# Optimization experiments

Measured on AMD Instinct MI355X. Metric: run time of the kernel, lower is better.

Reference implementation:

```python
import jax, jax.numpy as jnp
import numpy as np

D_STATE = 16
DT_RANK = 48
D_CONV = 4
EPS = 1e-5


def rmsnorm(x, w):
    return x * jax.lax.rsqrt(jnp.mean(x * x, axis=-1, keepdims=True) + EPS) * w


def causal_dw_conv(u, w, b):
    # u: [B,T,D], w: [D,K] depthwise causal kernel, b: [D]
    B, T, D = u.shape
    K = w.shape[1]
    up = jnp.pad(u, ((0, 0), (K - 1, 0), (0, 0)))
    acc = jnp.zeros_like(u)
    for k in range(K):  # K=4, tiny fixed loop
        acc = acc + up[:, k:k + T, :] * w[:, k]
    return acc + b


def mamba_mixer(h, ipw, cw, cb, xpw, dpw, dpb, alog, dpar, opw):
    # h: [B,T,d_model]
    B, T, _ = h.shape
    xz = h @ ipw.T                       # [B,T,2*d_inner]
    u, z = jnp.split(xz, 2, axis=-1)     # each [B,T,d_inner]
    u = jax.nn.silu(causal_dw_conv(u, cw, cb))
    xp = u @ xpw.T                       # [B,T,dt_rank+2*d_state]
    dt = xp[..., :DT_RANK]
    Bm = xp[..., DT_RANK:DT_RANK + D_STATE]
    Cm = xp[..., DT_RANK + D_STATE:]
    delta = jax.nn.softplus(dt @ dpw.T + dpb)      # [B,T,d_inner]
    A = -jnp.exp(alog)                              # [d_inner, d_state], negative
    dA = jnp.exp(delta[..., None] * A)              # [B,T,d_inner,d_state] in (0,1)
    dBu = (delta * u)[..., None] * Bm[:, :, None, :]
    # time-major for scan
    dA_t = jnp.moveaxis(dA, 1, 0)
    dBu_t = jnp.moveaxis(dBu, 1, 0)
    C_t = jnp.moveaxis(Cm, 1, 0)

    def step(hst, inp):
        a, bu, c = inp
        hst = a * hst + bu                          # [B,d_inner,d_state]
        y = jnp.einsum('bdn,bn->bd', hst, c)
        return hst, y

    h0 = jnp.zeros((B, u.shape[-1], D_STATE), u.dtype)
    _, ys = jax.lax.scan(step, h0, (dA_t, dBu_t, C_t))
    y = jnp.moveaxis(ys, 0, 1) + u * dpar           # skip via D
    y = y * jax.nn.silu(z)                          # gate
    return y @ opw.T                                # [B,T,d_model]


def setup_inputs() -> dict:
    key = jax.random.key(0)
    ks = jax.random.split(key, 16)
    L, d_model, d_inner = 4, 768, 1536
    B, C, T = 4, 256, 512
    s = 0.02
    return {
        'x': jax.random.normal(ks[0], (B, C, T), jnp.float32),
        'in_proj_w': jax.random.normal(ks[1], (L, 2 * d_inner, d_model), jnp.float32) * s,
        'conv_w': jax.random.normal(ks[2], (L, d_inner, D_CONV), jnp.float32) * 0.3,
        'conv_b': jnp.zeros((L, d_inner), jnp.float32),
        'x_proj_w': jax.random.normal(ks[3], (L, DT_RANK + 2 * D_STATE, d_inner), jnp.float32) * s,
        'dt_proj_w': jax.random.normal(ks[4], (L, d_inner, DT_RANK), jnp.float32) * 0.1,
        'dt_proj_b': jax.random.normal(ks[5], (L, d_inner), jnp.float32) * 0.1 - 4.0,
        'A_log': jax.random.uniform(ks[6], (L, d_inner, D_STATE), jnp.float32, 0.0, 1.5),
        'D_param': jax.random.uniform(ks[7], (L, d_inner), jnp.float32),
        'out_proj_w': jax.random.normal(ks[8], (L, d_model, d_inner), jnp.float32) * s,
        'norm_w': jnp.ones((L, d_model), jnp.float32),
        'norm_f_w': jnp.ones((d_model,), jnp.float32),
        'inp_w': jax.random.normal(ks[9], (d_model, C), jnp.float32) * s,
        'inp_b': jnp.zeros((d_model,), jnp.float32),
        'cls_w': jax.random.normal(ks[10], (10, d_model), jnp.float32) * s,
        'cls_b': jnp.zeros((10,), jnp.float32),
    }


def reference(x, in_proj_w, conv_w, conv_b, x_proj_w, dt_proj_w, dt_proj_b,
              A_log, D_param, out_proj_w, norm_w, norm_f_w,
              inp_w, inp_b, cls_w, cls_b):
    # x: (B, C, T) -> (B, T, C)
    xt = jnp.transpose(x, (0, 2, 1))
    h = xt @ inp_w.T + inp_b                # [B,T,d_model]
    hidden = h
    residual = None
    L = in_proj_w.shape[0]
    for l in range(L):
        residual = hidden if residual is None else hidden + residual
        normed = rmsnorm(residual, norm_w[l])
        hidden = mamba_mixer(normed, in_proj_w[l], conv_w[l], conv_b[l],
                             x_proj_w[l], dt_proj_w[l], dt_proj_b[l],
                             A_log[l], D_param[l], out_proj_w[l])
    residual = hidden + residual
    hidden = rmsnorm(residual, norm_f_w)
    pooled = hidden.mean(axis=1)            # [B,d_model]
    logits = pooled @ cls_w.T + cls_b       # [B,num_labels]
    return logits
```

## Files before the change

kernel.cpp:

```cpp
#include <hip/hip_runtime.h>
#include <math.h>

#define D_MODEL 768
#define D_INNER 1536
#define B_SZ 4
#define T_SZ 512
#define ROWS (B_SZ*T_SZ)
#define XP_N 80
#define CH 16
#define CT 32
#define XS 8
#define XKC (D_INNER/XS)
#define OS 4
#define OKC (D_INNER/OS)
#define MN_OUT (ROWS*768)

typedef __attribute__((ext_vector_type(8))) short bf16x8;
typedef __attribute__((ext_vector_type(4))) float f32x4;

#define GLL(g, l) __builtin_amdgcn_global_load_lds( \
    (const __attribute__((address_space(1))) void*)(g), \
    (__attribute__((address_space(3))) void*)(l), 16, 0, 0)

__device__ __forceinline__ float sigmoidf_(float x){ return 1.0f/(1.0f+__expf(-x)); }
__device__ __forceinline__ float siluf_(float x){ return x*sigmoidf_(x); }
__device__ __forceinline__ unsigned short f2bf(float f){
  unsigned u = __builtin_bit_cast(unsigned, f);
  u = (u + 0x7FFFu + ((u >> 16) & 1u)) >> 16;
  return (unsigned short)u;
}
__device__ __forceinline__ float bf2f(unsigned short v){
  return __builtin_bit_cast(float, (unsigned)v << 16);
}
__device__ __forceinline__ ushort4 cvt4(float4 v){
  ushort4 r; r.x=f2bf(v.x); r.y=f2bf(v.y); r.z=f2bf(v.z); r.w=f2bf(v.w); return r;
}

#define CA_N0 9437184LL
#define CA_N1 4718592LL
#define CA_N2 196608LL
#define CA_N3 786432LL
#define CA_N4 393216LL
__global__ __launch_bounds__(256) void cast_all(
    const float* __restrict__ ipw, unsigned short* __restrict__ wbi,
    const float* __restrict__ opw, unsigned short* __restrict__ wbo,
    const float* __restrict__ inpw, unsigned short* __restrict__ inpwb,
    const float* __restrict__ xpw, unsigned short* __restrict__ xpwb,
    const float* __restrict__ dtw, unsigned short* __restrict__ dtwb)
{
  long long i4 = ((long long)blockIdx.x*256 + threadIdx.x)*4;
  if (i4 < CA_N0){ *(ushort4*)(wbi + i4) = cvt4(*(const float4*)(ipw + i4)); return; }
  i4 -= CA_N0;
  if (i4 < CA_N1){ *(ushort4*)(wbo + i4) = cvt4(*(const float4*)(opw + i4)); return; }
  i4 -= CA_N1;
  if (i4 < CA_N2){ *(ushort4*)(inpwb + i4) = cvt4(*(const float4*)(inpw + i4)); return; }
  i4 -= CA_N2;
  if (i4 < CA_N3){
    const long long l = i4 / (128*1536), rem = i4 % (128*1536);
    const long long r = rem / 1536, k = rem % 1536;
    ushort4 o;
    if (r < 80) o = cvt4(*(const float4*)(xpw + (l*80 + r)*1536 + k));
    else { o.x=0;o.y=0;o.z=0;o.w=0; }
    *(ushort4*)(xpwb + i4) = o; return;
  }
  i4 -= CA_N3;
  if (i4 < CA_N4){
    const long long l = i4 / (1536*64), rem = i4 % (1536*64);
    const long long r = rem / 64, c = rem % 64;
    ushort4 o;
    if (c < 48) o = cvt4(*(const float4*)(dtw + (l*1536 + r)*48 + c));
    else { o.x=0;o.y=0;o.z=0;o.w=0; }
    *(ushort4*)(dtwb + i4) = o;
  }
}

__global__ void transpose_x(const float* __restrict__ x, unsigned short* __restrict__ xtb){
  __shared__ float s[32][33];
  int b = blockIdx.z;
  int t0 = blockIdx.x*32, c0 = blockIdx.y*32;
  int tx = threadIdx.x, ty = threadIdx.y;
  s[ty][tx] = x[((size_t)b*256 + (c0+ty))*512 + (t0+tx)];
  __syncthreads();
  xtb[((size_t)b*512 + (t0+ty))*256 + (c0+tx)] = f2bf(s[tx][ty]);
}

__global__ __launch_bounds__(256) void gemm_input(
    const unsigned short* __restrict__ A, const unsigned short* __restrict__ Wb,
    const float* __restrict__ bias, float* __restrict__ C)
{
  __shared__ unsigned short As[128*32];
  __shared__ unsigned short Ws[128*32];
  const int tid = threadIdx.x;
  const int bm = blockIdx.y*128, bn = blockIdx.x*128;
  const int wave = tid >> 6, lane = tid & 63;
  const int wm = (wave >> 1)*64, wn = (wave & 1)*64;
  const int fr = lane & 15, quad = lane >> 4;
  f32x4 acc[4][4] = {};
  const int row0 = (wave*64 + lane) >> 2;
  const int khl  = ((lane & 3) + 4 - ((row0 >> 1) & 3)) & 3;
  const unsigned short* Ag = A  + (size_t)(bm + row0)*256 + khl*8;
  const unsigned short* Wg = Wb + (size_t)(bn + row0)*256 + khl*8;
  const size_t rstep = (size_t)64*256;
  unsigned short* ldsA = As + wave*512;
  unsigned short* ldsW = Ws + wave*512;
  for (int k0 = 0; k0 < 256; k0 += 32){
    GLL(Ag + k0,          ldsA);
    GLL(Ag + rstep + k0,  ldsA + 2048);
    GLL(Wg + k0,          ldsW);
    GLL(Wg + rstep + k0,  ldsW + 2048);
    __syncthreads();
    bf16x8 a[4], b[4];
    #pragma unroll
    for (int i=0;i<4;i++){
      const int row = wm + i*16 + fr;
      a[i] = *(const bf16x8*)(As + row*32 + (((quad + (row>>1)) & 3)*8));
    }
    #pragma unroll
    for (int j=0;j<4;j++){
      const int row = wn + j*16 + fr;
      b[j] = *(const bf16x8*)(Ws + row*32 + (((quad + (row>>1)) & 3)*8));
    }
    #pragma unroll
    for (int i=0;i<4;i++)
      #pragma unroll
      for (int j=0;j<4;j++)
        acc[i][j] = __builtin_amdgcn_mfma_f32_16x16x32_bf16(a[i], b[j], acc[i][j], 0, 0, 0);
    __syncthreads();
  }
  #pragma unroll
  for (int i=0;i<4;i++)
    #pragma unroll
    for (int r=0;r<4;r++){
      const int row = bm + wm + i*16 + quad*4 + r;
      #pragma unroll
      for (int j=0;j<4;j++){
        const int col = bn + wn + j*16 + fr;
        C[(size_t)row*768 + col] = acc[i][j][r] + bias[col];
      }
    }
}

__global__ __launch_bounds__(256) void gemm_inproj(
    const unsigned short* __restrict__ A, const unsigned short* __restrict__ Wb,
    unsigned short* __restrict__ Cb)
{
  __shared__ unsigned short As[128*32];
  __shared__ unsigned short Ws[128*32];
  const int tid = threadIdx.x;
  const int bm = blockIdx.y*128, bn = blockIdx.x*128;
  const int wave = tid >> 6, lane = tid & 63;
  const int wm = (wave >> 1)*64, wn = (wave & 1)*64;
  const int fr = lane & 15, quad = lane >> 4;
  f32x4 acc[4][4] = {};
  const int row0 = (wave*64 + lane) >> 2;
  const int khl  = ((lane & 3) + 4 - ((row0 >> 1) & 3)) & 3;
  const unsigned short* Ag = A  + (size_t)(bm + row0)*768 + khl*8;
  const unsigned short* Wg = Wb + (size_t)(bn + row0)*768 + khl*8;
  const size_t rstep = (size_t)64*768;
  unsigned short* ldsA = As + wave*512;
  unsigned short* ldsW = Ws + wave*512;
  for (int k0 = 0; k0 < 768; k0 += 32){
    GLL(Ag + k0,          ldsA);
    GLL(Ag + rstep + k0,  ldsA + 2048);
    GLL(Wg + k0,          ldsW);
    GLL(Wg + rstep + k0,  ldsW + 2048);
    __syncthreads();
    bf16x8 a[4], b[4];
    #pragma unroll
    for (int i=0;i<4;i++){
      const int row = wm + i*16 + fr;
      a[i] = *(const bf16x8*)(As + row*32 + (((quad + (row>>1)) & 3)*8));
    }
    #pragma unroll
    for (int j=0;j<4;j++){
      const int row = wn + j*16 + fr;
      b[j] = *(const bf16x8*)(Ws + row*32 + (((quad + (row>>1)) & 3)*8));
    }
    #pragma unroll
    for (int i=0;i<4;i++)
      #pragma unroll
      for (int j=0;j<4;j++)
        acc[i][j] = __builtin_amdgcn_mfma_f32_16x16x32_bf16(a[i], b[j], acc[i][j], 0, 0, 0);
    __syncthreads();
  }
  #pragma unroll
  for (int i=0;i<4;i++)
    #pragma unroll
    for (int r=0;r<4;r++){
      const int row = bm + wm + i*16 + quad*4 + r;
      #pragma unroll
      for (int j=0;j<4;j++){
        const int col = bn + wn + j*16 + fr;
        Cb[(size_t)row*3072 + col] = f2bf(acc[i][j][r]);
      }
    }
}

__global__ __launch_bounds__(256) void gemm_xp_fused(
    const unsigned short* __restrict__ xzb, const float* __restrict__ cw,
    const float* __restrict__ cb, const unsigned short* __restrict__ Wl,
    float* __restrict__ part)
{
  __shared__ unsigned short AsAll[6*128*32];
  __shared__ unsigned short Ws[128*32];
  const int tid = threadIdx.x;
  const int bm = blockIdx.x*128;
  const int s  = blockIdx.y;
  const int koff = s*XKC;
  for (int task = tid; task < 128*24; task += 256){
    const int rl = task / 24, c8 = task % 24;
    const int r = bm + rl;
    const int t = r & (T_SZ-1);
    const int d0 = koff + c8*8;
    float acc[8];
    float4 cb0 = *(const float4*)(cb + d0);
    float4 cb1 = *(const float4*)(cb + d0 + 4);
    acc[0]=cb0.x; acc[1]=cb0.y; acc[2]=cb0.z; acc[3]=cb0.w;
    acc[4]=cb1.x; acc[5]=cb1.y; acc[6]=cb1.z; acc[7]=cb1.w;
    float4 cwv[8];
    #pragma unroll
    for (int j=0;j<8;j++) cwv[j] = *(const float4*)(cw + (size_t)(d0+j)*4);
    #pragma unroll
    for (int k=0;k<4;k++){
      const int tt = t - 3 + k;
      if (tt >= 0){
        bf16x8 xv = *(const bf16x8*)(xzb + (size_t)(r-3+k)*3072 + d0);
        #pragma unroll
        for (int j=0;j<8;j++)
          acc[j] += bf2f((unsigned short)xv[j]) * ((const float*)&cwv[j])[k];
      }
    }
    bf16x8 ov;
    #pragma unroll
    for (int j=0;j<8;j++) ov[j] = (short)f2bf(siluf_(acc[j]));
    const int kk = c8 >> 2, khl = c8 & 3;
    const int khp = (khl + (rl >> 1)) & 3;
    *(bf16x8*)(AsAll + kk*4096 + rl*32 + khp*8) = ov;
  }
  const int wave = tid >> 6, lane = tid & 63;
  const int wm = (wave >> 1)*64, wn = (wave & 1)*64;
  const int fr = lane & 15, quad = lane >> 4;
  const int row0 = (wave*64 + lane) >> 2;
  const int khl2 = ((lane & 3) + 4 - ((row0 >> 1) & 3)) & 3;
  const unsigned short* Wg = Wl + (size_t)row0*D_INNER + koff + khl2*8;
  const size_t rstepW = (size_t)64*D_INNER;
  unsigned short* ldsW = Ws + wave*512;
  f32x4 accm[4][4] = {};
  for (int k0 = 0; k0 < XKC; k0 += 32){
    GLL(Wg + k0,           ldsW);
    GLL(Wg + rstepW + k0,  ldsW + 2048);
    __syncthreads();
    const unsigned short* Ak = AsAll + (k0 >> 5)*4096;
    bf16x8 a[4], b[4];
    #pragma unroll
    for (int i=0;i<4;i++){
      const int row = wm + i*16 + fr;
      a[i] = *(const bf16x8*)(Ak + row*32 + (((quad + (row>>1)) & 3)*8));
    }
    #pragma unroll
    for (int j=0;j<4;j++){
      const int row = wn + j*16 + fr;
      b[j] = *(const bf16x8*)(Ws + row*32 + (((quad + (row>>1)) & 3)*8));
    }
    #pragma unroll
    for (int i=0;i<4;i++)
      #pragma unroll
      for (int j=0;j<4;j++)
        accm[i][j] = __builtin_amdgcn_mfma_f32_16x16x32_bf16(a[i], b[j], accm[i][j], 0, 0, 0);
    __syncthreads();
  }
  #pragma unroll
  for (int i=0;i<4;i++)
    #pragma unroll
    for (int r=0;r<4;r++){
      const int row = bm + wm + i*16 + quad*4 + r;
      #pragma unroll
      for (int j=0;j<4;j++){
        const int col = wn + j*16 + fr;
        if (col < XP_N)
          part[((size_t)s*ROWS + row)*XP_N + col] = accm[i][j][r];
      }
    }
}

__global__ __launch_bounds__(256) void gemm_dt_fused(
    const float* __restrict__ xpart, const unsigned short* __restrict__ Wl,
    const float* __restrict__ bias, float* __restrict__ xp, float* __restrict__ delta)
{
  __shared__ unsigned short AsAll[2*128*32];
  __shared__ unsigned short Ws[128*32];
  const int tid = threadIdx.x;
  const int bn = blockIdx.x*128, bm = blockIdx.y*128;
  {
    bf16x8 zv = {0,0,0,0,0,0,0,0};
    for (int i = tid; i < 1024; i += 256) *(bf16x8*)(AsAll + i*8) = zv;
  }
  __syncthreads();
  for (int task = tid; task < 128*10; task += 256){
    const int rl = task / 10, c8 = task % 10;
    const int row = bm + rl;
    const int col0 = c8*8;
    float4 sa = make_float4(0.f,0.f,0.f,0.f), sb = make_float4(0.f,0.f,0.f,0.f);
    #pragma unroll
    for (int k=0;k<XS;k++){
      const float* pp = xpart + ((size_t)k*ROWS + row)*XP_N + col0;
      float4 a = *(const float4*)pp;
      float4 b = *(const float4*)(pp + 4);
      sa.x+=a.x; sa.y+=a.y; sa.z+=a.z; sa.w+=a.w;
      sb.x+=b.x; sb.y+=b.y; sb.z+=b.z; sb.w+=b.w;
    }
    if (c8 < 6){
      bf16x8 ov;
      ov[0]=(short)f2bf(sa.x); ov[1]=(short)f2bf(sa.y); ov[2]=(short)f2bf(sa.z); ov[3]=(short)f2bf(sa.w);
      ov[4]=(short)f2bf(sb.x); ov[5]=(short)f2bf(sb.y); ov[6]=(short)f2bf(sb.z); ov[7]=(short)f2bf(sb.w);
      const int kk = c8 >> 2, khl = c8 & 3;
      const int khp = (khl + (rl >> 1)) & 3;
      *(bf16x8*)(AsAll + kk*4096 + rl*32 + khp*8) = ov;
    }
    if (bn == 0){
      *(float4*)(xp + (size_t)row*XP_N + col0)     = sa;
      *(float4*)(xp + (size_t)row*XP_N + col0 + 4) = sb;
    }
  }
  const int wave = tid >> 6, lane = tid & 63;
  const int wm = (wave >> 1)*64, wn = (wave & 1)*64;
  const int fr = lane & 15, quad = lane >> 4;
  const int row0 = (wave*64 + lane) >> 2;
  const int khl2 = ((lane & 3) + 4 - ((row0 >> 1) & 3)) & 3;
  const unsigned short* Wg = Wl + (size_t)(bn + row0)*64 + khl2*8;
  const size_t rstepW = (size_t)64*64;
  unsigned short* ldsW = Ws + wave*512;
  f32x4 accm[4][4] = {};
  for (int k0 = 0; k0 < 64; k0 += 32){
    GLL(Wg + k0,           ldsW);
    GLL(Wg + rstepW + k0,  ldsW + 2048);
    __syncthreads();
    const unsigned short* Ak = AsAll + (k0 >> 5)*4096;
    bf16x8 a[4], b[4];
    #pragma unroll
    for (int i=0;i<4;i++){
      const int row = wm + i*16 + fr;
      a[i] = *(const bf16x8*)(Ak + row*32 + (((quad + (row>>1)) & 3)*8));
    }
    #pragma unroll
    for (int j=0;j<4;j++){
      const int row = wn + j*16 + fr;
      b[j] = *(const bf16x8*)(Ws + row*32 + (((quad + (row>>1)) & 3)*8));
    }
    #pragma unroll
    for (int i=0;i<4;i++)
      #pragma unroll
      for (int j=0;j<4;j++)
        accm[i][j] = __builtin_amdgcn_mfma_f32_16x16x32_bf16(a[i], b[j], accm[i][j], 0, 0, 0);
    __syncthreads();
  }
  #pragma unroll
  for (int i=0;i<4;i++)
    #pragma unroll
    for (int r=0;r<4;r++){
      const int row = bm + wm + i*16 + quad*4 + r;
      float* Cp = delta + (size_t)row*D_INNER + bn + wn + fr;
      #pragma unroll
      for (int j=0;j<4;j++){
        const int col = bn + wn + j*16 + fr;
        float v = accm[i][j][r] + bias[col];
        v = (v > 20.f) ? v : log1pf(__expf(v));
        Cp[j*16] = v;
      }
    }
}

__global__ __launch_bounds__(256) void gemm_bf16_sk(
    const unsigned short* __restrict__ A, const unsigned short* __restrict__ Wb,
    float* __restrict__ P0, float* __restrict__ P1)
{
  __shared__ unsigned short As[128*32];
  __shared__ unsigned short Ws[128*32];
  const int tid = threadIdx.x;
  const int bm = blockIdx.y*128, bn = blockIdx.x*128;
  const int s = blockIdx.z;
  const int koff = s*OKC;
  const int wave = tid >> 6, lane = tid & 63;
  const int wm = (wave >> 1)*64, wn = (wave & 1)*64;
  const int fr = lane & 15, quad = lane >> 4;
  f32x4 acc[4][4] = {};
  const int row0 = (wave*64 + lane) >> 2;
  const int khl  = ((lane & 3) + 4 - ((row0 >> 1) & 3)) & 3;
  const unsigned short* Ag = A  + (size_t)(bm + row0)*1536 + koff + khl*8;
  const unsigned short* Wg = Wb + (size_t)(bn + row0)*1536 + koff + khl*8;
  const size_t rstep = (size_t)64*1536;
  unsigned short* ldsA = As + wave*512;
  unsigned short* ldsW = Ws + wave*512;
  for (int k0 = 0; k0 < OKC; k0 += 32){
    GLL(Ag + k0,          ldsA);
    GLL(Ag + rstep + k0,  ldsA + 2048);
    GLL(Wg + k0,          ldsW);
    GLL(Wg + rstep + k0,  ldsW + 2048);
    __syncthreads();
    bf16x8 a[4], b[4];
    #pragma unroll
    for (int i=0;i<4;i++){
      const int row = wm + i*16 + fr;
      a[i] = *(const bf16x8*)(As + row*32 + (((quad + (row>>1)) & 3)*8));
    }
    #pragma unroll
    for (int j=0;j<4;j++){
      const int row = wn + j*16 + fr;
      b[j] = *(const bf16x8*)(Ws + row*32 + (((quad + (row>>1)) & 3)*8));
    }
    #pragma unroll
    for (int i=0;i<4;i++)
      #pragma unroll
      for (int j=0;j<4;j++)
        acc[i][j] = __builtin_amdgcn_mfma_f32_16x16x32_bf16(a[i], b[j], acc[i][j], 0, 0, 0);
    __syncthreads();
  }
  float* Cbuf = (s < 2 ? P0 : P1) + (size_t)(s & 1)*MN_OUT;
  #pragma unroll
  for (int i=0;i<4;i++)
    #pragma unroll
    for (int r=0;r<4;r++){
      const int row = bm + wm + i*16 + quad*4 + r;
      float* Cp = Cbuf + (size_t)row*768 + bn + wn + fr;
      #pragma unroll
      for (int j=0;j<4;j++)
        Cp[j*16] = acc[i][j][r];
    }
}

__global__ __launch_bounds__(256) void fused_norm(
    float* __restrict__ resid, const float* __restrict__ P0, const float* __restrict__ P1,
    const float* __restrict__ w, unsigned short* __restrict__ obf, float* __restrict__ ofp)
{
  const int row = blockIdx.x;
  const int tid = threadIdx.x;
  float v[3];
  float ss = 0.f;
  #pragma unroll
  for (int i=0;i<3;i++){
    const int c = tid + i*256;
    const size_t idx = (size_t)row*768 + c;
    float r = resid[idx];
    if (P0) r += (P0[idx] + P0[MN_OUT + idx]) + (P1[idx] + P1[MN_OUT + idx]);
    v[i] = r;
    ss += r*r;
  }
  #pragma unroll
  for (int off=32; off>=1; off>>=1) ss += __shfl_xor(ss, off);
  __shared__ float sred[4];
  const int lane = tid & 63, wv = tid >> 6;
  if (lane == 0) sred[wv] = ss;
  __syncthreads();
  const float tot = sred[0]+sred[1]+sred[2]+sred[3];
  const float scale = rsqrtf(tot*(1.0f/768.0f) + 1e-5f);
  #pragma unroll
  for (int i=0;i<3;i++){
    const int c = tid + i*256;
    const size_t idx = (size_t)row*768 + c;
    if (P0) resid[idx] = v[i];
    const float o = v[i]*scale*w[c];
    if (obf) obf[idx] = f2bf(o);
    else     ofp[idx] = o;
  }
}

__global__ __launch_bounds__(256) void scan_pass1(
    const float* __restrict__ delta, const unsigned short* __restrict__ xzb,
    const float* __restrict__ cw, const float* __restrict__ cb,
    const float* __restrict__ xp, const float* __restrict__ alog,
    float* __restrict__ Pend, float* __restrict__ Hend)
{
  const int d = blockIdx.x*256 + threadIdx.x;
  const int b = blockIdx.y, c = blockIdx.z;
  float4 t0v = *(const float4*)(alog + d*16 + 0);
  float4 t1v = *(const float4*)(alog + d*16 + 4);
  float4 t2v = *(const float4*)(alog + d*16 + 8);
  float4 t3v = *(const float4*)(alog + d*16 + 12);
  float Av[16] = {t0v.x,t0v.y,t0v.z,t0v.w,t1v.x,t1v.y,t1v.z,t1v.w,
                  t2v.x,t2v.y,t2v.z,t2v.w,t3v.x,t3v.y,t3v.z,t3v.w};
  float h[16], P[16];
  #pragma unroll
  for (int n=0;n<16;n++){ Av[n] = -__expf(Av[n]); h[n]=0.f; P[n]=1.f; }
  const float4 cwv = *(const float4*)(cw + (size_t)d*4);
  const float cbd = cb[d];
  const size_t row0 = (size_t)b*T_SZ + (size_t)c*CT;
  const float* dp = delta + row0*D_INNER + d;
  const float* bp = xp    + row0*XP_N + 48;
  const unsigned short* xzp = xzb + row0*3072 + d;
  float xm3 = (c > 0) ? bf2f(xzp[-3*3072]) : 0.f;
  float xm2 = (c > 0) ? bf2f(xzp[-2*3072]) : 0.f;
  float xm1 = (c > 0) ? bf2f(xzp[-1*3072]) : 0.f;
  for (int t=0;t<CT;t++){
    const float dv = dp[(size_t)t*D_INNER];
    const float xc = bf2f(xzp[(size_t)t*3072]);
    float ac = cbd;
    ac += xm3*cwv.x; ac += xm2*cwv.y; ac += xm1*cwv.z; ac += xc*cwv.w;
    const float uv = siluf_(ac);
    xm3 = xm2; xm2 = xm1; xm1 = xc;
    const float4 B0 = *(const float4*)(bp + (size_t)t*XP_N);
    const float4 B1 = *(const float4*)(bp + (size_t)t*XP_N + 4);
    const float4 B2 = *(const float4*)(bp + (size_t)t*XP_N + 8);
    const float4 B3 = *(const float4*)(bp + (size_t)t*XP_N + 12);
    const float Bv[16] = {B0.x,B0.y,B0.z,B0.w,B1.x,B1.y,B1.z,B1.w,
                          B2.x,B2.y,B2.z,B2.w,B3.x,B3.y,B3.z,B3.w};
    const float du = dv*uv;
    #pragma unroll
    for (int n=0;n<16;n++){
      const float dA = __expf(dv*Av[n]);
      P[n] *= dA;
      h[n] = dA*h[n] + du*Bv[n];
    }
  }
  float* Pp = Pend + ((size_t)(b*CH+c)*D_INNER + d)*16;
  float* Hp = Hend + ((size_t)(b*CH+c)*D_INNER + d)*16;
  *(float4*)(Pp+ 0) = make_float4(P[0],P[1],P[2],P[3]);
  *(float4*)(Pp+ 4) = make_float4(P[4],P[5],P[6],P[7]);
  *(float4*)(Pp+ 8) = make_float4(P[8],P[9],P[10],P[11]);
  *(float4*)(Pp+12) = make_float4(P[12],P[13],P[14],P[15]);
  *(float4*)(Hp+ 0) = make_float4(h[0],h[1],h[2],h[3]);
  *(float4*)(Hp+ 4) = make_float4(h[4],h[5],h[6],h[7]);
  *(float4*)(Hp+ 8) = make_float4(h[8],h[9],h[10],h[11]);
  *(float4*)(Hp+12) = make_float4(h[12],h[13],h[14],h[15]);
}

__global__ __launch_bounds__(256) void scan_pass3(
    const float* __restrict__ delta, const unsigned short* __restrict__ xzb,
    const float* __restrict__ cw, const float* __restrict__ cb,
    const float* __restrict__ xp, const float* __restrict__ alog,
    const float* __restrict__ Dp, const float* __restrict__ Pend,
    const float* __restrict__ Hend, unsigned short* __restrict__ yb)
{
  const int d = blockIdx.x*256 + threadIdx.x;
  const int b = blockIdx.y, c = blockIdx.z;
  float4 t0v = *(const float4*)(alog + d*16 + 0);
  float4 t1v = *(const float4*)(alog + d*16 + 4);
  float4 t2v = *(const float4*)(alog + d*16 + 8);
  float4 t3v = *(const float4*)(alog + d*16 + 12);
  float Av[16] = {t0v.x,t0v.y,t0v.z,t0v.w,t1v.x,t1v.y,t1v.z,t1v.w,
                  t2v.x,t2v.y,t2v.z,t2v.w,t3v.x,t3v.y,t3v.z,t3v.w};
  float h[16];
  #pragma unroll
  for (int n=0;n<16;n++){ Av[n] = -__expf(Av[n]); h[n] = 0.f; }
  for (int cc=0; cc<c; cc++){
    const float* Pp = Pend + ((size_t)(b*CH+cc)*D_INNER + d)*16;
    const float* Hp = Hend + ((size_t)(b*CH+cc)*D_INNER + d)*16;
    float4 p0 = *(const float4*)(Pp+0),  p1 = *(const float4*)(Pp+4);
    float4 p2 = *(const float4*)(Pp+8),  p3 = *(const float4*)(Pp+12);
    float4 q0 = *(const float4*)(Hp+0),  q1 = *(const float4*)(Hp+4);
    float4 q2 = *(const float4*)(Hp+8),  q3 = *(const float4*)(Hp+12);
    const float Pv[16] = {p0.x,p0.y,p0.z,p0.w,p1.x,p1.y,p1.z,p1.w,
                          p2.x,p2.y,p2.z,p2.w,p3.x,p3.y,p3.z,p3.w};
    const float Hv[16] = {q0.x,q0.y,q0.z,q0.w,q1.x,q1.y,q1.z,q1.w,
                          q2.x,q2.y,q2.z,q2.w,q3.x,q3.y,q3.z,q3.w};
    #pragma unroll
    for (int n=0;n<16;n++) h[n] = Pv[n]*h[n] + Hv[n];
  }
  const float Dv = Dp[d];
  const float4 cwv = *(const float4*)(cw + (size_t)d*4);
  const float cbd = cb[d];
  const size_t row0 = (size_t)b*T_SZ + (size_t)c*CT;
  const float* dp = delta + row0*D_INNER + d;
  const float* bp = xp    + row0*XP_N + 48;
  const float* cp = xp    + row0*XP_N + 64;
  const unsigned short* xzp = xzb + row0*3072 + d;
  const unsigned short* zp  = xzb + row0*3072 + 1536 + d;
  unsigned short* yp = yb + row0*D_INNER + d;
  float xm3 = (c > 0) ? bf2f(xzp[-3*3072]) : 0.f;
  float xm2 = (c > 0) ? bf2f(xzp[-2*3072]) : 0.f;
  float xm1 = (c > 0) ? bf2f(xzp[-1*3072]) : 0.f;
  for (int t=0;t<CT;t++){
    const float dv = dp[(size_t)t*D_INNER];
    const float xc = bf2f(xzp[(size_t)t*3072]);
    float ac = cbd;
    ac += xm3*cwv.x; ac += xm2*cwv.y; ac += xm1*cwv.z; ac += xc*cwv.w;
    const float uv = siluf_(ac);
    xm3 = xm2; xm2 = xm1; xm1 = xc;
    const float zv = bf2f(zp[(size_t)t*3072]);
    const float4 B0 = *(const float4*)(bp + (size_t)t*XP_N);
    const float4 B1 = *(const float4*)(bp + (size_t)t*XP_N + 4);
    const float4 B2 = *(const float4*)(bp + (size_t)t*XP_N + 8);
    const float4 B3 = *(const float4*)(bp + (size_t)t*XP_N + 12);
    const float4 C0 = *(const float4*)(cp + (size_t)t*XP_N);
    const float4 C1 = *(const float4*)(cp + (size_t)t*XP_N + 4);
    const float4 C2 = *(const float4*)(cp + (size_t)t*XP_N + 8);
    const float4 C3 = *(const float4*)(cp + (size_t)t*XP_N + 12);
    const float Bv[16] = {B0.x,B0.y,B0.z,B0.w,B1.x,B1.y,B1.z,B1.w,
                          B2.x,B2.y,B2.z,B2.w,B3.x,B3.y,B3.z,B3.w};
    const float Cv[16] = {C0.x,C0.y,C0.z,C0.w,C1.x,C1.y,C1.z,C1.w,
                          C2.x,C2.y,C2.z,C2.w,C3.x,C3.y,C3.z,C3.w};
    const float du = dv*uv;
    float p = 0.f;
    #pragma unroll
    for (int n=0;n<16;n++){
      const float dA = __expf(dv*Av[n]);
      h[n] = dA*h[n] + du*Bv[n];
      p += h[n]*Cv[n];
    }
    yp[(size_t)t*D_INNER] = f2bf((p + uv*Dv)*siluf_(zv));
  }
}

__global__ __launch_bounds__(256) void pool_partial(const float* __restrict__ normed,
                                                    float* __restrict__ part){
  const int i = blockIdx.x*256 + threadIdx.x;
  const int s = blockIdx.y;
  const int b = i / 768, m = i % 768;
  float sum = 0.f;
  const float* p = normed + ((size_t)b*T_SZ + s*32)*768 + m;
  #pragma unroll
  for (int t=0; t<32; t++) sum += p[(size_t)t*768];
  part[s*3072 + i] = sum;
}

__global__ __launch_bounds__(256) void pool_cls(const float* __restrict__ part,
                                                const float* __restrict__ cw,
                                                const float* __restrict__ cb,
                                                float* __restrict__ out){
  __shared__ float ls[768];
  const int b = blockIdx.x;
  const int tid = threadIdx.x;
  #pragma unroll
  for (int i=0;i<3;i++){
    const int m = tid + i*256;
    float s = 0.f;
    #pragma unroll
    for (int c=0;c<16;c++) s += part[c*3072 + b*768 + m];
    ls[m] = s * (1.0f/T_SZ);
  }
  __syncthreads();
  const int wave = tid >> 6, lane = tid & 63;
  for (int o = wave; o < 10; o += 4){
    float s = 0.f;
    for (int k = lane; k < 768; k += 64) s += ls[k]*cw[o*768 + k];
    #pragma unroll
    for (int off=32; off>=1; off>>=1) s += __shfl_xor(s, off);
    if (lane == 0) out[b*10 + o] = s + cb[o];
  }
}

extern "C" void kernel_launch(void* const* d_in, const int* in_sizes, int n_in,
                              void* d_out, int out_size, void* d_ws, size_t ws_size,
                              hipStream_t stream) {
  const float* x         = (const float*)d_in[0];
  const float* in_proj_w = (const float*)d_in[1];
  const float* conv_w    = (const float*)d_in[2];
  const float* conv_b    = (const float*)d_in[3];
  const float* x_proj_w  = (const float*)d_in[4];
  const float* dt_proj_w = (const float*)d_in[5];
  const float* dt_proj_b = (const float*)d_in[6];
  const float* A_log     = (const float*)d_in[7];
  const float* D_param   = (const float*)d_in[8];
  const float* out_proj_w= (const float*)d_in[9];
  const float* norm_w    = (const float*)d_in[10];
  const float* norm_f_w  = (const float*)d_in[11];
  const float* inp_w     = (const float*)d_in[12];
  const float* inp_b     = (const float*)d_in[13];
  const float* cls_w     = (const float*)d_in[14];
  const float* cls_b     = (const float*)d_in[15];
  float* out = (float*)d_out;

  char* ws = (char*)d_ws;
  auto carve = [&](size_t nelem)->float* {
    float* p = (float*)ws;
    ws += ((nelem*sizeof(float) + 255)/256)*256;
    return p;
  };
  float* xtb_f  = carve((size_t)ROWS*256/2);
  float* resid  = carve((size_t)ROWS*768);
  float* normed = carve((size_t)ROWS*768);
  float* hidden = carve((size_t)ROWS*768);
  float* xzb_f  = carve((size_t)ROWS*3072/2);
  float* pbuf2  = carve((size_t)ROWS*1536);
  float* xp     = carve((size_t)ROWS*XP_N);
  float* delta  = carve((size_t)ROWS*1536);
  float* ybf_f  = carve((size_t)ROWS*1536/2);
  float* wbi_f  = carve((size_t)CA_N0/2);
  float* wbo_f  = carve((size_t)CA_N1/2);
  float* wip_f  = carve((size_t)CA_N2/2);
  float* wxp_f  = carve((size_t)CA_N3/2);
  float* wdt_f  = carve((size_t)CA_N4/2);
  float* xpart  = carve((size_t)XS*ROWS*XP_N);
  float* ppool  = carve((size_t)16*3072);

  unsigned short* xtb = (unsigned short*)xtb_f;
  unsigned short* normedb = (unsigned short*)normed;
  unsigned short* xzb = (unsigned short*)xzb_f;
  unsigned short* ybf = (unsigned short*)ybf_f;
  unsigned short* wbi = (unsigned short*)wbi_f;
  unsigned short* wbo = (unsigned short*)wbo_f;
  unsigned short* wip = (unsigned short*)wip_f;
  unsigned short* wxp = (unsigned short*)wxp_f;
  unsigned short* wdt = (unsigned short*)wdt_f;
  float* Pend = normed;
  float* Hend = hidden;

  cast_all<<<15168, 256, 0, stream>>>(in_proj_w, wbi, out_proj_w, wbo,
                                      inp_w, wip, x_proj_w, wxp, dt_proj_w, wdt);
  transpose_x<<<dim3(16,8,4), dim3(32,32), 0, stream>>>(x, xtb);
  gemm_input<<<dim3(6,16), 256, 0, stream>>>(xtb, wip, inp_b, resid);

  for (int l = 0; l < 4; l++){
    fused_norm<<<2048, 256, 0, stream>>>(resid, l ? delta : nullptr, l ? pbuf2 : nullptr,
                                         norm_w + (size_t)l*768, normedb, nullptr);
    gemm_inproj<<<dim3(24,16), 256, 0, stream>>>(normedb, wbi + (size_t)l*3072*768, xzb);
    gemm_xp_fused<<<dim3(16,XS), 256, 0, stream>>>(xzb, conv_w + (size_t)l*1536*4,
                                                   conv_b + (size_t)l*1536,
                                                   wxp + (size_t)l*128*1536, xpart);
    gemm_dt_fused<<<dim3(12,16), 256, 0, stream>>>(xpart, wdt + (size_t)l*1536*64,
                                                   dt_proj_b + (size_t)l*1536, xp, delta);
    scan_pass1<<<dim3(6,B_SZ,CH-1), 256, 0, stream>>>(delta, xzb,
                                                      conv_w + (size_t)l*1536*4,
                                                      conv_b + (size_t)l*1536, xp,
                                                      A_log + (size_t)l*1536*16, Pend, Hend);
    scan_pass3<<<dim3(6,B_SZ,CH), 256, 0, stream>>>(delta, xzb,
                                                    conv_w + (size_t)l*1536*4,
                                                    conv_b + (size_t)l*1536, xp,
                                                    A_log + (size_t)l*1536*16,
                                                    D_param + (size_t)l*1536, Pend, Hend, ybf);
    gemm_bf16_sk<<<dim3(6,16,OS), 256, 0, stream>>>(ybf, wbo + (size_t)l*768*1536,
                                                    delta, pbuf2);
  }

  fused_norm<<<2048, 256, 0, stream>>>(resid, delta, pbuf2, norm_f_w, nullptr, normed);
  pool_partial<<<dim3(12,16), 256, 0, stream>>>(normed, ppool);
  pool_cls<<<4, 256, 0, stream>>>(ppool, cls_w, cls_b, out);
}
```

Measured before the change: 876.2 us.

## Split conv+SiLU out of x_proj GEMM and double its split-K factor

```diff
diff --git a/kernel.cpp b/kernel.cpp
--- a/kernel.cpp
+++ b/kernel.cpp
@@ -9,7 +9,7 @@
 #define XP_N 80
 #define CH 16
 #define CT 32
-#define XS 8
+#define XS 16
 #define XKC (D_INNER/XS)
 #define OS 4
 #define OKC (D_INNER/OS)
@@ -196,66 +196,57 @@
     }
 }
 
-__global__ __launch_bounds__(256) void gemm_xp_fused(
+__global__ __launch_bounds__(256) void conv_silu(
     const unsigned short* __restrict__ xzb, const float* __restrict__ cw,
-    const float* __restrict__ cb, const unsigned short* __restrict__ Wl,
+    const float* __restrict__ cb, unsigned short* __restrict__ ub)
+{
+  const int idx = blockIdx.x*256 + threadIdx.x;
+  if (idx >= ROWS*D_INNER) return;
+  const int d = idx % D_INNER;
+  const int row = idx / D_INNER;
+  const int t = row & (T_SZ-1);
+  float acc = cb[d];
+  #pragma unroll
+  for (int k=0;k<4;k++){
+    const int tt = t - 3 + k;
+    if (tt >= 0)
+      acc += bf2f(xzb[(size_t)(row - 3 + k)*3072 + d]) * cw[d*4 + k];
+  }
+  ub[idx] = f2bf(siluf_(acc));
+}
+
+__global__ __launch_bounds__(256) void gemm_bf16_xp(
+    const unsigned short* __restrict__ A, const unsigned short* __restrict__ Wb,
     float* __restrict__ part)
 {
-  __shared__ unsigned short AsAll[6*128*32];
+  __shared__ unsigned short As[128*32];
   __shared__ unsigned short Ws[128*32];
   const int tid = threadIdx.x;
   const int bm = blockIdx.x*128;
-  const int s  = blockIdx.y;
+  const int s = blockIdx.y;
   const int koff = s*XKC;
-  for (int task = tid; task < 128*24; task += 256){
-    const int rl = task / 24, c8 = task % 24;
-    const int r = bm + rl;
-    const int t = r & (T_SZ-1);
-    const int d0 = koff + c8*8;
-    float acc[8];
-    float4 cb0 = *(const float4*)(cb + d0);
-    float4 cb1 = *(const float4*)(cb + d0 + 4);
-    acc[0]=cb0.x; acc[1]=cb0.y; acc[2]=cb0.z; acc[3]=cb0.w;
-    acc[4]=cb1.x; acc[5]=cb1.y; acc[6]=cb1.z; acc[7]=cb1.w;
-    float4 cwv[8];
-    #pragma unroll
-    for (int j=0;j<8;j++) cwv[j] = *(const float4*)(cw + (size_t)(d0+j)*4);
-    #pragma unroll
-    for (int k=0;k<4;k++){
-      const int tt = t - 3 + k;
-      if (tt >= 0){
-        bf16x8 xv = *(const bf16x8*)(xzb + (size_t)(r-3+k)*3072 + d0);
-        #pragma unroll
-        for (int j=0;j<8;j++)
-          acc[j] += bf2f((unsigned short)xv[j]) * ((const float*)&cwv[j])[k];
-      }
-    }
-    bf16x8 ov;
-    #pragma unroll
-    for (int j=0;j<8;j++) ov[j] = (short)f2bf(siluf_(acc[j]));
-    const int kk = c8 >> 2, khl = c8 & 3;
-    const int khp = (khl + (rl >> 1)) & 3;
-    *(bf16x8*)(AsAll + kk*4096 + rl*32 + khp*8) = ov;
-  }
   const int wave = tid >> 6, lane = tid & 63;
   const int wm = (wave >> 1)*64, wn = (wave & 1)*64;
   const int fr = lane & 15, quad = lane >> 4;
+  f32x4 acc[4][4] = {};
   const int row0 = (wave*64 + lane) >> 2;
-  const int khl2 = ((lane & 3) + 4 - ((row0 >> 1) & 3)) & 3;
-  const unsigned short* Wg = Wl + (size_t)row0*D_INNER + koff + khl2*8;
-  const size_t rstepW = (size_t)64*D_INNER;
+  const int khl  = ((lane & 3) + 4 - ((row0 >> 1) & 3)) & 3;
+  const unsigned short* Ag = A  + (size_t)(bm + row0)*D_INNER + koff + khl*8;
+  const unsigned short* Wg = Wb + (size_t)row0*D_INNER + koff + khl*8;
+  const size_t rstep = (size_t)64*D_INNER;
+  unsigned short* ldsA = As + wave*512;
   unsigned short* ldsW = Ws + wave*512;
-  f32x4 accm[4][4] = {};
   for (int k0 = 0; k0 < XKC; k0 += 32){
-    GLL(Wg + k0,           ldsW);
-    GLL(Wg + rstepW + k0,  ldsW + 2048);
-    __syncthreads();
-    const unsigned short* Ak = AsAll + (k0 >> 5)*4096;
+    GLL(Ag + k0,          ldsA);
+    GLL(Ag + rstep + k0,  ldsA + 2048);
+    GLL(Wg + k0,          ldsW);
+    GLL(Wg + rstep + k0,  ldsW + 2048);
+    __syncthreads();
     bf16x8 a[4], b[4];
     #pragma unroll
     for (int i=0;i<4;i++){
       const int row = wm + i*16 + fr;
-      a[i] = *(const bf16x8*)(Ak + row*32 + (((quad + (row>>1)) & 3)*8));
+      a[i] = *(const bf16x8*)(As + row*32 + (((quad + (row>>1)) & 3)*8));
     }
     #pragma unroll
     for (int j=0;j<4;j++){
@@ -266,7 +257,7 @@
     for (int i=0;i<4;i++)
       #pragma unroll
       for (int j=0;j<4;j++)
-        accm[i][j] = __builtin_amdgcn_mfma_f32_16x16x32_bf16(a[i], b[j], accm[i][j], 0, 0, 0);
+        acc[i][j] = __builtin_amdgcn_mfma_f32_16x16x32_bf16(a[i], b[j], acc[i][j], 0, 0, 0);
     __syncthreads();
   }
   #pragma unroll
@@ -278,7 +269,7 @@
       for (int j=0;j<4;j++){
         const int col = wn + j*16 + fr;
         if (col < XP_N)
-          part[((size_t)s*ROWS + row)*XP_N + col] = accm[i][j][r];
+          part[((size_t)s*ROWS + row)*XP_N + col] = acc[i][j][r];
       }
     }
 }
@@ -674,6 +665,7 @@
   float* xp     = carve((size_t)ROWS*XP_N);
   float* delta  = carve((size_t)ROWS*1536);
   float* ybf_f  = carve((size_t)ROWS*1536/2);
+  float* ubf_f  = carve((size_t)ROWS*1536/2);
   float* wbi_f  = carve((size_t)CA_N0/2);
   float* wbo_f  = carve((size_t)CA_N1/2);
   float* wip_f  = carve((size_t)CA_N2/2);
@@ -686,6 +678,7 @@
   unsigned short* normedb = (unsigned short*)normed;
   unsigned short* xzb = (unsigned short*)xzb_f;
   unsigned short* ybf = (unsigned short*)ybf_f;
+  unsigned short* ubf = (unsigned short*)ubf_f;
   unsigned short* wbi = (unsigned short*)wbi_f;
   unsigned short* wbo = (unsigned short*)wbo_f;
   unsigned short* wip = (unsigned short*)wip_f;
@@ -703,9 +696,9 @@
     fused_norm<<<2048, 256, 0, stream>>>(resid, l ? delta : nullptr, l ? pbuf2 : nullptr,
                                          norm_w + (size_t)l*768, normedb, nullptr);
     gemm_inproj<<<dim3(24,16), 256, 0, stream>>>(normedb, wbi + (size_t)l*3072*768, xzb);
-    gemm_xp_fused<<<dim3(16,XS), 256, 0, stream>>>(xzb, conv_w + (size_t)l*1536*4,
-                                                   conv_b + (size_t)l*1536,
-                                                   wxp + (size_t)l*128*1536, xpart);
+    conv_silu<<<(ROWS*D_INNER)/256, 256, 0, stream>>>(xzb, conv_w + (size_t)l*1536*4,
+                                                      conv_b + (size_t)l*1536, ubf);
+    gemm_bf16_xp<<<dim3(16,XS), 256, 0, stream>>>(ubf, wxp + (size_t)l*128*1536, xpart);
     gemm_dt_fused<<<dim3(12,16), 256, 0, stream>>>(xpart, wdt + (size_t)l*1536*64,
                                                    dt_proj_b + (size_t)l*1536, xp, delta);
     scan_pass1<<<dim3(6,B_SZ,CH-1), 256, 0, stream>>>(delta, xzb,
```

New measurement: 838.3 us. -4.3%, faster.
